# Kernel optimization log

Measured on AMD Instinct MI355X. Metric: run time of the kernel, lower is better.

## Reference

```python
import jax, jax.numpy as jnp
import numpy as np

B, T, D = 2, 2048, 2048
H, K, Hd = 16, 8, 128
EPS = 1e-6
THETA = 1e6


def _rms_norm(x, w):
    # x: [..., Hd]
    return x * jax.lax.rsqrt(jnp.mean(x * x, axis=-1, keepdims=True) + EPS) * w


def _rope(x, sin, cos):
    # x: [B, T, Hh, Hd]; sin/cos: [T, Hd//2]
    s = sin[None, :, None, :]
    c = cos[None, :, None, :]
    x1 = x[..., 0::2]
    x2 = x[..., 1::2]
    # NOTE: source concatenates halves (non-interleaved output), replicate exactly
    return jnp.concatenate([x1 * c - x2 * s, x1 * s + x2 * c], axis=-1)


def setup_inputs() -> dict:
    key = jax.random.key(0)
    ks = jax.random.split(key, 5)
    scale = 0.02
    x = jax.random.normal(ks[0], (B, T, D), dtype=jnp.float32)
    Wq = jax.random.normal(ks[1], (D, H * Hd), dtype=jnp.float32) * scale
    Wk = jax.random.normal(ks[2], (D, K * Hd), dtype=jnp.float32) * scale
    Wv = jax.random.normal(ks[3], (D, K * Hd), dtype=jnp.float32) * scale
    Wo = jax.random.normal(ks[4], (H * Hd, D), dtype=jnp.float32) * scale
    qn_w = jnp.ones((Hd,), dtype=jnp.float32)
    kn_w = jnp.ones((Hd,), dtype=jnp.float32)
    # RotaryEmbedding: inv_freq = theta**(-arange(0,Hd,2)/Hd); freqs = outer(t, inv_freq)
    inv_freq = 1.0 / (THETA ** (jnp.arange(0, Hd, 2, dtype=jnp.float32) / Hd))
    freqs = jnp.arange(T, dtype=jnp.float32)[:, None] * inv_freq[None, :]
    return {"x": x, "Wq": Wq, "Wk": Wk, "Wv": Wv, "Wo": Wo,
            "qn_w": qn_w, "kn_w": kn_w,
            "sin": jnp.sin(freqs), "cos": jnp.cos(freqs)}


def reference(x, Wq, Wk, Wv, Wo, qn_w, kn_w, sin, cos):
    Bx, Tx, _ = x.shape
    q = (x @ Wq).reshape(Bx, Tx, H, Hd)
    k = (x @ Wk).reshape(Bx, Tx, K, Hd)
    v = (x @ Wv).reshape(Bx, Tx, K, Hd)
    q = _rope(_rms_norm(q, qn_w), sin, cos)
    k = _rope(_rms_norm(k, kn_w), sin, cos)
    q = q.transpose(0, 2, 1, 3)  # [B,H,T,Hd]
    k = k.transpose(0, 2, 1, 3)  # [B,K,T,Hd]
    v = v.transpose(0, 2, 1, 3)
    if K != 1 and K != H:
        rep = H // K
        k = jnp.repeat(k, rep, axis=1)  # repeat_interleave on head dim
        v = jnp.repeat(v, rep, axis=1)
    att = jnp.einsum('bhqd,bhkd->bhqk', q.astype(jnp.float32),
                     k.astype(jnp.float32)) / np.sqrt(Hd).astype(np.float32)
    causal = jnp.tril(jnp.ones((Tx, Tx), dtype=bool))
    att = jnp.where(causal[None, None], att, -jnp.inf)
    att = jax.nn.softmax(att, axis=-1)
    out = jnp.einsum('bhqk,bhkd->bhqd', att, v.astype(jnp.float32))
    out = out.astype(q.dtype).transpose(0, 2, 1, 3).reshape(Bx, Tx, H * Hd)
    return out @ Wo
```

## Files before the change

kernel.cpp:

```cpp
#include <hip/hip_runtime.h>
#include <stdint.h>


#define B_ 2
#define T_ 2048
#define D_ 2048
#define H_ 16
#define KH_ 8
#define HD_ 128
#define M_ (B_*T_)
#define NQKV_ 4096
#define QK_SCALE_LOG2E 0.1275174337f

typedef unsigned short u16;
typedef unsigned int   u32;
typedef __attribute__((ext_vector_type(8))) __bf16 bf16x8_t;
typedef __attribute__((ext_vector_type(4))) float  f32x4_t;

__device__ __forceinline__ u16 f2bf(float f) {
    u32 x = __float_as_uint(f);
    return (u16)((x + 0x7fffu + ((x >> 16) & 1u)) >> 16);
}
__device__ __forceinline__ u32 pack2(u16 a, u16 b) { return (u32)a | ((u32)b << 16); }

__device__ __forceinline__ void gload16(const void* g, void* l) {
    __builtin_amdgcn_global_load_lds(
        (__attribute__((address_space(1))) const void*)(unsigned long long)g,
        (__attribute__((address_space(3))) void*)(u32)(unsigned long long)l,
        16, 0, 0);
}

__global__ void cast_x_kernel(const float* __restrict__ in, u16* __restrict__ out) {
    int i = (blockIdx.x * 256 + threadIdx.x) * 4;
    float4 v = *(const float4*)(in + i);
    u32 lo = pack2(f2bf(v.x), f2bf(v.y));
    u32 hi = pack2(f2bf(v.z), f2bf(v.w));
    *(uint2*)(out + i) = make_uint2(lo, hi);
}

__global__ void tcast_kernel(const float* __restrict__ in, u16* __restrict__ out,
                             int ncols) {
    __shared__ u16 tile[64][65];
    int k0 = blockIdx.x * 64;
    int n0 = blockIdx.y * 64;
    int tid = threadIdx.x;
#pragma unroll
    for (int i = 0; i < 8; ++i) {
        int idx = tid + i * 256;
        int r = idx >> 5, c2 = idx & 31;
        float2 v = *(const float2*)(in + (size_t)(k0 + r) * ncols + n0 + 2 * c2);
        tile[r][2 * c2]     = f2bf(v.x);
        tile[r][2 * c2 + 1] = f2bf(v.y);
    }
    __syncthreads();
#pragma unroll
    for (int i = 0; i < 8; ++i) {
        int idx = tid + i * 256;
        int rn = idx >> 5, c2 = idx & 31;
        *(u32*)(out + (size_t)(n0 + rn) * 2048 + k0 + 2 * c2) =
            pack2(tile[2 * c2][rn], tile[2 * c2 + 1][rn]);
    }
}

__global__ void __launch_bounds__(256)
gemm_kernel(const u16* __restrict__ A, const u16* __restrict__ Bt,
            float* __restrict__ C, int N) {
    __shared__ u16 As[128 * 32];
    __shared__ u16 Bs[128 * 32];
    const int tid  = threadIdx.x;
    const int lane = tid & 63;
    const int wid  = tid >> 6;
    const int m0 = blockIdx.x * 128;
    const int n0 = blockIdx.y * 128;

    const int c0 = wid * 2, c1 = wid * 2 + 1;
    const int r0 = c0 * 16 + (lane >> 2);
    const int r1 = c1 * 16 + (lane >> 2);
    const int cl = lane & 3;
    const int g0 = cl ^ ((r0 >> 1) & 3);
    const int g1 = cl ^ ((r1 >> 1) & 3);
    const u16* gA0 = A  + (size_t)(m0 + r0) * 2048 + g0 * 8;
    const u16* gA1 = A  + (size_t)(m0 + r1) * 2048 + g1 * 8;
    const u16* gB0 = Bt + (size_t)(n0 + r0) * 2048 + g0 * 8;
    const u16* gB1 = Bt + (size_t)(n0 + r1) * 2048 + g1 * 8;
    u16* lA0 = As + c0 * 512;
    u16* lA1 = As + c1 * 512;
    u16* lB0 = Bs + c0 * 512;
    u16* lB1 = Bs + c1 * 512;

    const int wm = (wid >> 1) * 64, wn = (wid & 1) * 64;
    const int fr  = lane & 15;
    const int kg  = lane >> 4;

    f32x4_t acc[4][4];
#pragma unroll
    for (int m = 0; m < 4; ++m)
#pragma unroll
        for (int n = 0; n < 4; ++n)
#pragma unroll
            for (int j = 0; j < 4; ++j) acc[m][n][j] = 0.0f;

    for (int ks = 0; ks < 64; ++ks) {
        gload16(gA0, lA0); gload16(gA1, lA1);
        gload16(gB0, lB0); gload16(gB1, lB1);
        gA0 += 32; gA1 += 32; gB0 += 32; gB1 += 32;
        __syncthreads();
        bf16x8_t af[4], bfv[4];
#pragma unroll
        for (int m = 0; m < 4; ++m) {
            int row = wm + m * 16 + fr;
            int phys = kg ^ ((row >> 1) & 3);
            af[m] = *(const bf16x8_t*)(As + row * 32 + phys * 8);
        }
#pragma unroll
        for (int n = 0; n < 4; ++n) {
            int row = wn + n * 16 + fr;
            int phys = kg ^ ((row >> 1) & 3);
            bfv[n] = *(const bf16x8_t*)(Bs + row * 32 + phys * 8);
        }
#pragma unroll
        for (int m = 0; m < 4; ++m)
#pragma unroll
            for (int n = 0; n < 4; ++n)
                acc[m][n] = __builtin_amdgcn_mfma_f32_16x16x32_bf16(
                    af[m], bfv[n], acc[m][n], 0, 0, 0);
        __syncthreads();
    }

#pragma unroll
    for (int m = 0; m < 4; ++m)
#pragma unroll
        for (int n = 0; n < 4; ++n) {
            int col   = n0 + wn + n * 16 + fr;
            int rbase = m0 + wm + m * 16 + kg * 4;
#pragma unroll
            for (int j = 0; j < 4; ++j)
                C[(size_t)(rbase + j) * N + col] = acc[m][n][j];
        }
}

__global__ void __launch_bounds__(256)
normrope_kernel(const float* __restrict__ Cqkv,
                const float* __restrict__ qw, const float* __restrict__ kw,
                const float* __restrict__ sinT, const float* __restrict__ cosT,
                u16* __restrict__ qbf, u16* __restrict__ kbf, u16* __restrict__ vbf) {
    int lane = threadIdx.x & 63;
    int w    = threadIdx.x >> 6;
    int rid  = blockIdx.x * 4 + w;
    int m   = rid >> 5;
    int sub = rid & 31;
    int b = m >> 11, t = m & (T_ - 1);

    if (sub >= 24) {
        int kh = sub - 24;
        float2 x = *(const float2*)(Cqkv + (size_t)m * NQKV_ + 3072 + kh * HD_ + 2 * lane);
        *(u32*)(vbf + ((size_t)(b * KH_ + kh) * T_ + t) * HD_ + 2 * lane) =
            pack2(f2bf(x.x), f2bf(x.y));
        return;
    }
    bool isq = sub < 16;
    int  hh  = isq ? sub : sub - 16;
    int  colbase = isq ? hh * HD_ : 2048 + hh * HD_;
    float2 x = *(const float2*)(Cqkv + (size_t)m * NQKV_ + colbase + 2 * lane);
    float ss = x.x * x.x + x.y * x.y;
#pragma unroll
    for (int sh = 1; sh < 64; sh <<= 1) ss += __shfl_xor(ss, sh, 64);
    float scale = rsqrtf(ss * (1.0f / 128.0f) + 1e-6f);
    const float* wp = isq ? qw : kw;
    float2 wv = *(const float2*)(wp + 2 * lane);
    float y1 = x.x * scale * wv.x;
    float y2 = x.y * scale * wv.y;
    float c = cosT[t * 64 + lane], s = sinT[t * 64 + lane];
    float oa = y1 * c - y2 * s;
    float ob = y1 * s + y2 * c;
    if (isq) { oa *= QK_SCALE_LOG2E; ob *= QK_SCALE_LOG2E; }
    u16* outp = isq ? (qbf + ((size_t)(b * H_  + hh) * T_ + t) * HD_)
                    : (kbf + ((size_t)(b * KH_ + hh) * T_ + t) * HD_);
    outp[lane]      = f2bf(oa);
    outp[64 + lane] = f2bf(ob);
}

__global__ void vtrans_kernel(const u16* __restrict__ in, u16* __restrict__ out) {
    __shared__ u16 tile[64][65];
    int t0 = blockIdx.x * 64;
    int d0 = blockIdx.y * 64;
    size_t bi = (size_t)blockIdx.z * T_ * HD_;
    size_t bo = (size_t)blockIdx.z * HD_ * T_;
    int tid = threadIdx.x;
#pragma unroll
    for (int i = 0; i < 8; ++i) {
        int idx = tid + i * 256;
        int r = idx >> 5, c2 = idx & 31;
        u32 v = *(const u32*)(in + bi + (size_t)(t0 + r) * HD_ + d0 + 2 * c2);
        tile[r][2 * c2]     = (u16)(v & 0xffffu);
        tile[r][2 * c2 + 1] = (u16)(v >> 16);
    }
    __syncthreads();
#pragma unroll
    for (int i = 0; i < 8; ++i) {
        int idx = tid + i * 256;
        int rd = idx >> 5, c2 = idx & 31;
        *(u32*)(out + bo + (size_t)(d0 + rd) * T_ + t0 + 2 * c2) =
            pack2(tile[2 * c2][rd], tile[2 * c2 + 1][rd]);
    }
}

__global__ void __launch_bounds__(256)
attn_kernel(const u16* __restrict__ qg, const u16* __restrict__ kgl,
            const u16* __restrict__ vtg, u16* __restrict__ attout) {
    __shared__ u16 Kt[64 * 128];
    __shared__ u16 Vt[128 * 64];
    __shared__ u16 Pb[4][16 * 72];

    const int tid = threadIdx.x, lane = tid & 63, w = tid >> 6;
    const int qb = blockIdx.x, h = blockIdx.y, b = blockIdx.z;
    const int kh = h >> 1;
    const int q0 = qb * 64;
    const u16* qbase = qg  + ((size_t)(b * H_  + h ) * T_) * HD_;
    const u16* kbase = kgl + ((size_t)(b * KH_ + kh) * T_) * HD_;
    const u16* vbase = vtg + ((size_t)(b * KH_ + kh) * HD_) * T_;

    const int fr  = lane & 15;
    const int kg4 = lane >> 4;
    const int qw0 = q0 + w * 16;

    bf16x8_t qf[4];
#pragma unroll
    for (int dblk = 0; dblk < 4; ++dblk)
        qf[dblk] = *(const bf16x8_t*)(qbase + (size_t)(qw0 + fr) * HD_ + dblk * 32 + kg4 * 8);

    const int krl = lane >> 4, kcl = lane & 15;
    const int vrl = lane >> 3, vcl = lane & 7;

    f32x4_t o[8];
#pragma unroll
    for (int dg = 0; dg < 8; ++dg)
#pragma unroll
        for (int j = 0; j < 4; ++j) o[dg][j] = 0.0f;
    float mrow[4], lrow[4];
#pragma unroll
    for (int j = 0; j < 4; ++j) { mrow[j] = -1e30f; lrow[j] = 0.0f; }

    const int nt = qb + 1;
    for (int t = 0; t < nt; ++t) {
        const int kv0 = t * 64;
#pragma unroll
        for (int cc = 0; cc < 4; ++cc) {
            int c = w * 4 + cc;
            int r = c * 4 + krl;
            int g = kcl ^ (r & 7);
            gload16(kbase + (size_t)(kv0 + r) * HD_ + g * 8, Kt + c * 512);
            int rv = c * 8 + vrl;
            int gv = vcl ^ (rv & 7);
            gload16(vbase + (size_t)rv * T_ + kv0 + gv * 8, Vt + c * 512);
        }
        __syncthreads();

        f32x4_t s[4];
#pragma unroll
        for (int cg = 0; cg < 4; ++cg) {
#pragma unroll
            for (int j = 0; j < 4; ++j) s[cg][j] = 0.0f;
#pragma unroll
            for (int dblk = 0; dblk < 4; ++dblk) {
                int row  = cg * 16 + fr;
                int phys = (dblk * 4 + kg4) ^ (row & 7);
                bf16x8_t kf = *(const bf16x8_t*)(Kt + row * 128 + phys * 8);
                s[cg] = __builtin_amdgcn_mfma_f32_16x16x32_bf16(qf[dblk], kf, s[cg], 0, 0, 0);
            }
        }
        if (t == nt - 1) {
#pragma unroll
            for (int cg = 0; cg < 4; ++cg) {
                int kv = kv0 + cg * 16 + fr;
#pragma unroll
                for (int j = 0; j < 4; ++j) {
                    int q = qw0 + kg4 * 4 + j;
                    if (kv > q) s[cg][j] = -1e30f;
                }
            }
        }
        float tm[4];
#pragma unroll
        for (int j = 0; j < 4; ++j)
            tm[j] = fmaxf(fmaxf(s[0][j], s[1][j]), fmaxf(s[2][j], s[3][j]));
#pragma unroll
        for (int sh = 1; sh < 16; sh <<= 1)
#pragma unroll
            for (int j = 0; j < 4; ++j)
                tm[j] = fmaxf(tm[j], __shfl_xor(tm[j], sh, 64));
        float corr[4];
#pragma unroll
        for (int j = 0; j < 4; ++j) {
            float mnew = fmaxf(mrow[j], tm[j]);
            corr[j] = exp2f(mrow[j] - mnew);
            mrow[j] = mnew;
        }
        float pr[4][4], rs[4] = {0.f, 0.f, 0.f, 0.f};
#pragma unroll
        for (int cg = 0; cg < 4; ++cg)
#pragma unroll
            for (int j = 0; j < 4; ++j) {
                float p = exp2f(s[cg][j] - mrow[j]);
                pr[cg][j] = p;
                rs[j] += p;
            }
#pragma unroll
        for (int sh = 1; sh < 16; sh <<= 1)
#pragma unroll
            for (int j = 0; j < 4; ++j) rs[j] += __shfl_xor(rs[j], sh, 64);
#pragma unroll
        for (int j = 0; j < 4; ++j) lrow[j] = lrow[j] * corr[j] + rs[j];
#pragma unroll
        for (int dg = 0; dg < 8; ++dg)
#pragma unroll
            for (int j = 0; j < 4; ++j) o[dg][j] *= corr[j];
#pragma unroll
        for (int cg = 0; cg < 4; ++cg)
#pragma unroll
            for (int j = 0; j < 4; ++j)
                Pb[w][(kg4 * 4 + j) * 72 + cg * 16 + fr] = f2bf(pr[cg][j]);
        bf16x8_t pa[2];
#pragma unroll
        for (int kvb = 0; kvb < 2; ++kvb)
            pa[kvb] = *(const bf16x8_t*)(&Pb[w][fr * 72 + kvb * 32 + kg4 * 8]);
#pragma unroll
        for (int dg = 0; dg < 8; ++dg) {
            int d = dg * 16 + fr;
#pragma unroll
            for (int kvb = 0; kvb < 2; ++kvb) {
                int phys = (kvb * 4 + kg4) ^ (d & 7);
                bf16x8_t vf = *(const bf16x8_t*)(Vt + d * 64 + phys * 8);
                o[dg] = __builtin_amdgcn_mfma_f32_16x16x32_bf16(pa[kvb], vf, o[dg], 0, 0, 0);
            }
        }
        __syncthreads();
    }
    float inv[4];
#pragma unroll
    for (int j = 0; j < 4; ++j) inv[j] = 1.0f / lrow[j];
    size_t rb = (size_t)(b * T_ + qw0);
#pragma unroll
    for (int dg = 0; dg < 8; ++dg)
#pragma unroll
        for (int j = 0; j < 4; ++j)
            attout[(rb + kg4 * 4 + j) * 2048 + h * HD_ + dg * 16 + fr] =
                f2bf(o[dg][j] * inv[j]);
}

extern "C" void kernel_launch(void* const* d_in, const int* in_sizes, int n_in,
                              void* d_out, int out_size, void* d_ws, size_t ws_size,
                              hipStream_t stream) {
    const float* x    = (const float*)d_in[0];
    const float* Wq   = (const float*)d_in[1];
    const float* Wk   = (const float*)d_in[2];
    const float* Wv   = (const float*)d_in[3];
    const float* Wo   = (const float*)d_in[4];
    const float* qw   = (const float*)d_in[5];
    const float* kw   = (const float*)d_in[6];
    const float* sinT = (const float*)d_in[7];
    const float* cosT = (const float*)d_in[8];
    float* out = (float*)d_out;

    u16*  x_bf   = (u16*)d_ws;
    u16*  wqkv_t = x_bf   + (size_t)M_ * D_;
    u16*  wo_t   = wqkv_t + (size_t)4096 * 2048;
    float* c_qkv = (float*)(wo_t + (size_t)2048 * 2048);
    u16*  q_bf   = (u16*)(c_qkv + (size_t)M_ * NQKV_);
    u16*  k_bf   = q_bf + (size_t)B_ * H_  * T_ * HD_;
    u16*  v_bf   = k_bf + (size_t)B_ * KH_ * T_ * HD_;
    u16*  v_t    = v_bf + (size_t)B_ * KH_ * T_ * HD_;
    u16*  att_bf = v_t  + (size_t)B_ * KH_ * T_ * HD_;

    cast_x_kernel<<<(M_ * D_) / 1024, 256, 0, stream>>>(x, x_bf);
    tcast_kernel<<<dim3(32, 32), 256, 0, stream>>>(Wq, wqkv_t, 2048);
    tcast_kernel<<<dim3(32, 16), 256, 0, stream>>>(Wk, wqkv_t + (size_t)2048 * 2048, 1024);
    tcast_kernel<<<dim3(32, 16), 256, 0, stream>>>(Wv, wqkv_t + (size_t)3072 * 2048, 1024);
    tcast_kernel<<<dim3(32, 32), 256, 0, stream>>>(Wo, wo_t, 2048);

    gemm_kernel<<<dim3(32, 32), 256, 0, stream>>>(x_bf, wqkv_t, c_qkv, 4096);
    normrope_kernel<<<(M_ * 32) / 4, 256, 0, stream>>>(c_qkv, qw, kw, sinT, cosT,
                                                       q_bf, k_bf, v_bf);
    vtrans_kernel<<<dim3(32, 2, 16), 256, 0, stream>>>(v_bf, v_t);
    attn_kernel<<<dim3(32, 16, 2), 256, 0, stream>>>(q_bf, k_bf, v_t, att_bf);
    gemm_kernel<<<dim3(32, 16), 256, 0, stream>>>(att_bf, wo_t, out, 2048);
}
```

Measured before the change: 491.5 us.

## Double-buffer K/V tiles in attention with 128-row query blocks and reversed scheduling

The attention kernel now uses 512 threads covering 128 query rows per block, and double-buffers the K and V tiles in shared memory. The next tile is prefetched while the current one is computed, with K and V loads split across separate warp groups. Blocks are launched heaviest-first by reversing the query-block index, per-warp causal skipping avoids fully masked tiles, and setprio raises priority around the MFMA sections. This doubles shared memory and halves the grid, which may reduce occupancy and parallelism across CUs.

```diff
diff --git a/kernel.cpp b/kernel.cpp
--- a/kernel.cpp
+++ b/kernel.cpp
@@ -205,17 +205,18 @@
     }
 }
 
-__global__ void __launch_bounds__(256)
+__global__ void __launch_bounds__(512)
 attn_kernel(const u16* __restrict__ qg, const u16* __restrict__ kgl,
             const u16* __restrict__ vtg, u16* __restrict__ attout) {
-    __shared__ u16 Kt[64 * 128];
-    __shared__ u16 Vt[128 * 64];
-    __shared__ u16 Pb[4][16 * 72];
+    __shared__ u16 Kt[2][64 * 128];
+    __shared__ u16 Vt[2][128 * 64];
+    __shared__ u16 Pb[8][16 * 72];
 
     const int tid = threadIdx.x, lane = tid & 63, w = tid >> 6;
-    const int qb = blockIdx.x, h = blockIdx.y, b = blockIdx.z;
+    const int qb = (int)gridDim.x - 1 - (int)blockIdx.x;
+    const int h = blockIdx.y, b = blockIdx.z;
     const int kh = h >> 1;
-    const int q0 = qb * 64;
+    const int q0 = qb * 128;
     const u16* qbase = qg  + ((size_t)(b * H_  + h ) * T_) * HD_;
     const u16* kbase = kgl + ((size_t)(b * KH_ + kh) * T_) * HD_;
     const u16* vbase = vtg + ((size_t)(b * KH_ + kh) * HD_) * T_;
@@ -241,101 +242,128 @@
 #pragma unroll
     for (int j = 0; j < 4; ++j) { mrow[j] = -1e30f; lrow[j] = 0.0f; }
 
-    const int nt = qb + 1;
+    const int nt = 2 * (qb + 1);
+
+#define STAGE(buf, tt)                                                         \
+    do {                                                                       \
+        int kv0s = (tt) * 64;                                                  \
+        if (w < 4) {                                                           \
+            _Pragma("unroll")                                                  \
+            for (int cc = 0; cc < 4; ++cc) {                                   \
+                int c = w * 4 + cc;                                            \
+                int r = c * 4 + krl;                                           \
+                int g = kcl ^ (r & 7);                                         \
+                gload16(kbase + (size_t)(kv0s + r) * HD_ + g * 8,              \
+                        &Kt[buf][c * 512]);                                    \
+            }                                                                  \
+        } else {                                                               \
+            _Pragma("unroll")                                                  \
+            for (int cc = 0; cc < 4; ++cc) {                                   \
+                int c = (w - 4) * 4 + cc;                                      \
+                int rv = c * 8 + vrl;                                          \
+                int gv = vcl ^ (rv & 7);                                       \
+                gload16(vbase + (size_t)rv * T_ + kv0s + gv * 8,               \
+                        &Vt[buf][c * 512]);                                    \
+            }                                                                  \
+        }                                                                      \
+    } while (0)
+
+    STAGE(0, 0);
+    __syncthreads();
+
     for (int t = 0; t < nt; ++t) {
+        const int cur = t & 1;
         const int kv0 = t * 64;
-#pragma unroll
-        for (int cc = 0; cc < 4; ++cc) {
-            int c = w * 4 + cc;
-            int r = c * 4 + krl;
-            int g = kcl ^ (r & 7);
-            gload16(kbase + (size_t)(kv0 + r) * HD_ + g * 8, Kt + c * 512);
-            int rv = c * 8 + vrl;
-            int gv = vcl ^ (rv & 7);
-            gload16(vbase + (size_t)rv * T_ + kv0 + gv * 8, Vt + c * 512);
+        if (t + 1 < nt) STAGE(cur ^ 1, t + 1);
+
+        if (kv0 <= qw0 + 15) {
+            f32x4_t s[4];
+            __builtin_amdgcn_s_setprio(1);
+#pragma unroll
+            for (int cg = 0; cg < 4; ++cg) {
+#pragma unroll
+                for (int j = 0; j < 4; ++j) s[cg][j] = 0.0f;
+#pragma unroll
+                for (int dblk = 0; dblk < 4; ++dblk) {
+                    int row  = cg * 16 + fr;
+                    int phys = (dblk * 4 + kg4) ^ (row & 7);
+                    bf16x8_t kf = *(const bf16x8_t*)(&Kt[cur][row * 128 + phys * 8]);
+                    s[cg] = __builtin_amdgcn_mfma_f32_16x16x32_bf16(qf[dblk], kf, s[cg], 0, 0, 0);
+                }
+            }
+            __builtin_amdgcn_s_setprio(0);
+            if (kv0 + 63 > qw0) {
+#pragma unroll
+                for (int cg = 0; cg < 4; ++cg) {
+                    int kv = kv0 + cg * 16 + fr;
+#pragma unroll
+                    for (int j = 0; j < 4; ++j) {
+                        int q = qw0 + kg4 * 4 + j;
+                        if (kv > q) s[cg][j] = -1e30f;
+                    }
+                }
+            }
+            float tm[4];
+#pragma unroll
+            for (int j = 0; j < 4; ++j)
+                tm[j] = fmaxf(fmaxf(s[0][j], s[1][j]), fmaxf(s[2][j], s[3][j]));
+#pragma unroll
+            for (int sh = 1; sh < 16; sh <<= 1)
+#pragma unroll
+                for (int j = 0; j < 4; ++j)
+                    tm[j] = fmaxf(tm[j], __shfl_xor(tm[j], sh, 64));
+            float corr[4];
+#pragma unroll
+            for (int j = 0; j < 4; ++j) {
+                float mnew = fmaxf(mrow[j], tm[j]);
+                corr[j] = exp2f(mrow[j] - mnew);
+                mrow[j] = mnew;
+            }
+            float pr[4][4], rs[4] = {0.f, 0.f, 0.f, 0.f};
+#pragma unroll
+            for (int cg = 0; cg < 4; ++cg)
+#pragma unroll
+                for (int j = 0; j < 4; ++j) {
+                    float p = exp2f(s[cg][j] - mrow[j]);
+                    pr[cg][j] = p;
+                    rs[j] += p;
+                }
+#pragma unroll
+            for (int sh = 1; sh < 16; sh <<= 1)
+#pragma unroll
+                for (int j = 0; j < 4; ++j) rs[j] += __shfl_xor(rs[j], sh, 64);
+#pragma unroll
+            for (int j = 0; j < 4; ++j) lrow[j] = lrow[j] * corr[j] + rs[j];
+#pragma unroll
+            for (int dg = 0; dg < 8; ++dg)
+#pragma unroll
+                for (int j = 0; j < 4; ++j) o[dg][j] *= corr[j];
+#pragma unroll
+            for (int cg = 0; cg < 4; ++cg)
+#pragma unroll
+                for (int j = 0; j < 4; ++j)
+                    Pb[w][(kg4 * 4 + j) * 72 + cg * 16 + fr] = f2bf(pr[cg][j]);
+            bf16x8_t pa[2];
+#pragma unroll
+            for (int kvb = 0; kvb < 2; ++kvb)
+                pa[kvb] = *(const bf16x8_t*)(&Pb[w][fr * 72 + kvb * 32 + kg4 * 8]);
+            __builtin_amdgcn_s_setprio(1);
+#pragma unroll
+            for (int dg = 0; dg < 8; ++dg) {
+                int d = dg * 16 + fr;
+#pragma unroll
+                for (int kvb = 0; kvb < 2; ++kvb) {
+                    int phys = (kvb * 4 + kg4) ^ (d & 7);
+                    bf16x8_t vf = *(const bf16x8_t*)(&Vt[cur][d * 64 + phys * 8]);
+                    o[dg] = __builtin_amdgcn_mfma_f32_16x16x32_bf16(pa[kvb], vf, o[dg], 0, 0, 0);
+                }
+            }
+            __builtin_amdgcn_s_setprio(0);
         }
         __syncthreads();
-
-        f32x4_t s[4];
-#pragma unroll
-        for (int cg = 0; cg < 4; ++cg) {
-#pragma unroll
-            for (int j = 0; j < 4; ++j) s[cg][j] = 0.0f;
-#pragma unroll
-            for (int dblk = 0; dblk < 4; ++dblk) {
-                int row  = cg * 16 + fr;
-                int phys = (dblk * 4 + kg4) ^ (row & 7);
-                bf16x8_t kf = *(const bf16x8_t*)(Kt + row * 128 + phys * 8);
-                s[cg] = __builtin_amdgcn_mfma_f32_16x16x32_bf16(qf[dblk], kf, s[cg], 0, 0, 0);
-            }
-        }
-        if (t == nt - 1) {
-#pragma unroll
-            for (int cg = 0; cg < 4; ++cg) {
-                int kv = kv0 + cg * 16 + fr;
-#pragma unroll
-                for (int j = 0; j < 4; ++j) {
-                    int q = qw0 + kg4 * 4 + j;
-                    if (kv > q) s[cg][j] = -1e30f;
-                }
-            }
-        }
-        float tm[4];
-#pragma unroll
-        for (int j = 0; j < 4; ++j)
-            tm[j] = fmaxf(fmaxf(s[0][j], s[1][j]), fmaxf(s[2][j], s[3][j]));
-#pragma unroll
-        for (int sh = 1; sh < 16; sh <<= 1)
-#pragma unroll
-            for (int j = 0; j < 4; ++j)
-                tm[j] = fmaxf(tm[j], __shfl_xor(tm[j], sh, 64));
-        float corr[4];
-#pragma unroll
-        for (int j = 0; j < 4; ++j) {
-            float mnew = fmaxf(mrow[j], tm[j]);
-            corr[j] = exp2f(mrow[j] - mnew);
-            mrow[j] = mnew;
-        }
-        float pr[4][4], rs[4] = {0.f, 0.f, 0.f, 0.f};
-#pragma unroll
-        for (int cg = 0; cg < 4; ++cg)
-#pragma unroll
-            for (int j = 0; j < 4; ++j) {
-                float p = exp2f(s[cg][j] - mrow[j]);
-                pr[cg][j] = p;
-                rs[j] += p;
-            }
-#pragma unroll
-        for (int sh = 1; sh < 16; sh <<= 1)
-#pragma unroll
-            for (int j = 0; j < 4; ++j) rs[j] += __shfl_xor(rs[j], sh, 64);
-#pragma unroll
-        for (int j = 0; j < 4; ++j) lrow[j] = lrow[j] * corr[j] + rs[j];
-#pragma unroll
-        for (int dg = 0; dg < 8; ++dg)
-#pragma unroll
-            for (int j = 0; j < 4; ++j) o[dg][j] *= corr[j];
-#pragma unroll
-        for (int cg = 0; cg < 4; ++cg)
-#pragma unroll
-            for (int j = 0; j < 4; ++j)
-                Pb[w][(kg4 * 4 + j) * 72 + cg * 16 + fr] = f2bf(pr[cg][j]);
-        bf16x8_t pa[2];
-#pragma unroll
-        for (int kvb = 0; kvb < 2; ++kvb)
-            pa[kvb] = *(const bf16x8_t*)(&Pb[w][fr * 72 + kvb * 32 + kg4 * 8]);
-#pragma unroll
-        for (int dg = 0; dg < 8; ++dg) {
-            int d = dg * 16 + fr;
-#pragma unroll
-            for (int kvb = 0; kvb < 2; ++kvb) {
-                int phys = (kvb * 4 + kg4) ^ (d & 7);
-                bf16x8_t vf = *(const bf16x8_t*)(Vt + d * 64 + phys * 8);
-                o[dg] = __builtin_amdgcn_mfma_f32_16x16x32_bf16(pa[kvb], vf, o[dg], 0, 0, 0);
-            }
-        }
-        __syncthreads();
-    }
+    }
+#undef STAGE
+
     float inv[4];
 #pragma unroll
     for (int j = 0; j < 4; ++j) inv[j] = 1.0f / lrow[j];
@@ -382,6 +410,6 @@
     normrope_kernel<<<(M_ * 32) / 4, 256, 0, stream>>>(c_qkv, qw, kw, sinT, cosT,
                                                        q_bf, k_bf, v_bf);
     vtrans_kernel<<<dim3(32, 2, 16), 256, 0, stream>>>(v_bf, v_t);
-    attn_kernel<<<dim3(32, 16, 2), 256, 0, stream>>>(q_bf, k_bf, v_t, att_bf);
+    attn_kernel<<<dim3(16, 16, 2), 512, 0, stream>>>(q_bf, k_bf, v_t, att_bf);
     gemm_kernel<<<dim3(32, 16), 256, 0, stream>>>(att_bf, wo_t, out, 2048);
 }
```

New measurement: 478.2 us. 2.7% less time.
